# Kernel optimization log

Measured on AMD Instinct MI355X. Metric: run time of the kernel, lower is better.

## Reference

```python
import jax, jax.numpy as jnp
import numpy as np

S = 4  # upsample scale


def setup_inputs() -> dict:
    key = jax.random.key(0)
    ks = jax.random.split(key, 8)
    B, C, H, W = 4, 128, 64, 64
    feat_lr = jax.random.normal(ks[0], (B, C, H, W), dtype=jnp.float32)
    # gate: Conv2d(C, C//4, 1, bias=False) -> LeakyReLU(0.2) -> Conv2d(C//4, 1, 1, bias=True) -> Sigmoid
    gate_w1 = jax.random.normal(ks[1], (C, C // 4), dtype=jnp.float32) * 0.05
    gate_w2 = jax.random.normal(ks[2], (C // 4, 1), dtype=jnp.float32) * 0.1
    gate_b2 = jnp.full((1,), -3.0, dtype=jnp.float32)  # init bias per module
    # mlp: Conv2d(C+2, C, 1) -> ReLU -> Conv2d(C, C, 1)
    mlp_w1 = jax.random.normal(ks[3], (C + 2, C), dtype=jnp.float32) * 0.05
    mlp_b1 = jax.random.normal(ks[4], (C,), dtype=jnp.float32) * 0.01
    mlp_w2 = jax.random.normal(ks[5], (C, C), dtype=jnp.float32) * 0.05
    mlp_b2 = jax.random.normal(ks[6], (C,), dtype=jnp.float32) * 0.01
    return {"feat_lr": feat_lr, "gate_w1": gate_w1, "gate_w2": gate_w2,
            "gate_b2": gate_b2, "mlp_w1": mlp_w1, "mlp_b1": mlp_b1,
            "mlp_w2": mlp_w2, "mlp_b2": mlp_b2}


def reference(feat_lr, gate_w1, gate_w2, gate_b2, mlp_w1, mlp_b1, mlp_w2, mlp_b2):
    B, C, H, W = feat_lr.shape
    f = jnp.transpose(feat_lr, (0, 2, 3, 1))  # (B,H,W,C)

    # ---- gate on LR grid (1x1 convs == per-pixel matmuls) ----
    g = f @ gate_w1                              # (B,H,W,C//4)
    g = jnp.where(g >= 0, g, 0.2 * g)            # LeakyReLU(0.2)
    gate = jax.nn.sigmoid(g @ gate_w2 + gate_b2) # (B,H,W,1)

    # ---- subpixel grid: channels [x, y], values in (-1,1) ----
    coords = jnp.linspace(-1.0 + 1.0 / S, 1.0 - 1.0 / S, S, dtype=feat_lr.dtype)
    yy, xx = jnp.meshgrid(coords, coords, indexing="ij")
    grid = jnp.stack([xx, yy], axis=-1)          # (S,S,2)

    # ---- mlp: split first conv weight into feat part and grid part.
    # Since convs are 1x1 and feat_hr is nearest-upsampled (constant over each
    # SxS block) while grid tiles per block, hidden = relu(f@W1f + grid@W1g + b1)
    # broadcast over (block, subpixel) — avoids materializing concat/HR inputs.
    w1_f, w1_g = mlp_w1[:C], mlp_w1[C:]          # (C,C), (2,C)
    h_f = f @ w1_f                               # (B,H,W,C)
    h_g = grid @ w1_g                            # (S,S,C)
    hidden = jax.nn.relu(h_f[:, :, None, :, None, :]
                         + h_g[None, None, :, None, :, :]
                         + mlp_b1)               # (B,H,S,W,S,C)
    res = hidden @ mlp_w2 + mlp_b2               # (B,H,S,W,S,C)

    out = res * gate[:, :, None, :, None, :]     # broadcast gate over block
    out = out.reshape(B, H * S, W * S, C)
    return jnp.transpose(out, (0, 3, 1, 2))      # (B,C,H*S,W*S)
```

## Files before the change

kernel.cpp:

```cpp
#include <hip/hip_runtime.h>
#include <hip/hip_bf16.h>
#include <math.h>


typedef __attribute__((ext_vector_type(8))) short bf16x8;
typedef __attribute__((ext_vector_type(4))) float f32x4;

__device__ inline short f2bf(float v) {
    __hip_bfloat16 b = __float2bfloat16(v);
    return *reinterpret_cast<short*>(&b);
}

__device__ inline void barrier_lgkm() {
    asm volatile("s_waitcnt lgkmcnt(0)" ::: "memory");
    __builtin_amdgcn_s_barrier();
    asm volatile("" ::: "memory");
}

__global__ __launch_bounds__(256) void ipi_pre_kernel(
    const float* __restrict__ w2,
    const float* __restrict__ w1,
    const float* __restrict__ gw1,
    __hip_bfloat16* __restrict__ w2t,
    __hip_bfloat16* __restrict__ w1t_hi,
    __hip_bfloat16* __restrict__ w1t_lo,
    __hip_bfloat16* __restrict__ g1t_hi,
    __hip_bfloat16* __restrict__ g1t_lo)
{
    int gid = blockIdx.x * 256 + threadIdx.x;
    if (gid < 16384) {
        int j = gid >> 7, k = gid & 127;
        w2t[gid] = __float2bfloat16(w2[k * 128 + j]);
    } else if (gid < 32768) {
        int i = gid - 16384, j = i >> 7, c = i & 127;
        float v = w1[c * 128 + j];
        __hip_bfloat16 hi = __float2bfloat16(v);
        w1t_hi[i] = hi;
        w1t_lo[i] = __float2bfloat16(v - __bfloat162float(hi));
    } else if (gid < 36864) {
        int i = gid - 32768, jg = i >> 7, c = i & 127;
        float v = gw1[c * 32 + jg];
        __hip_bfloat16 hi = __float2bfloat16(v);
        g1t_hi[i] = hi;
        g1t_lo[i] = __float2bfloat16(v - __bfloat162float(hi));
    }
}

__global__ __launch_bounds__(256, 4) void ipi_main(
    const float* __restrict__ feat,
    const float* __restrict__ mlp_w1,
    const float* __restrict__ mlp_b1,
    const float* __restrict__ gate_w2,
    const float* __restrict__ gate_b2,
    const float* __restrict__ mlp_b2,
    const __hip_bfloat16* __restrict__ w2t,
    const __hip_bfloat16* __restrict__ w1t_hi,
    const __hip_bfloat16* __restrict__ w1t_lo,
    const __hip_bfloat16* __restrict__ g1t_hi,
    const __hip_bfloat16* __restrict__ g1t_lo,
    float* __restrict__ out)
{
    __shared__ float hf_s[16 * 132];
    __shared__ float hgb_s[16 * 132];
    __shared__ float gate_s[16];
    __shared__ char  hid[16384];
    short* f_hi = (short*)hid;
    short* f_lo = (short*)(hid + 4352);
    float* glds = (float*)(hid + 8704);

    const int t    = threadIdx.x;
    const int lane = t & 63;
    const int lg   = lane >> 4;
    const int ml   = lane & 15;
    const int wv   = t >> 6;
    const int bx   = blockIdx.x;
    const int w0   = (bx & 3) * 16;
    const int h    = (bx >> 2) & 63;
    const int b    = bx >> 8;

    bf16x8 afrag[2][4];
    f32x4  b2v[2];
    {
        const __hip_bfloat16* base = w2t + (wv * 32 + ml) * 128 + lg * 8;
        #pragma unroll
        for (int jt = 0; jt < 2; ++jt) {
            #pragma unroll
            for (int ks = 0; ks < 4; ++ks)
                afrag[jt][ks] = *(const bf16x8*)(base + jt * 2048 + ks * 32);
            b2v[jt] = *(const f32x4*)&mlp_b2[wv * 32 + jt * 16 + lg * 4];
        }
    }

    {
        const float* fbase = feat + ((size_t)(b * 128) * 64 + h) * 64 + w0;
        #pragma unroll
        for (int i = 0; i < 8; ++i) {
            int idx = t + i * 256;
            int c = idx >> 4, w = idx & 15;
            float v = fbase[(size_t)c * 4096 + w];
            short hi = f2bf(v);
            float hf32 = __bfloat162float(*(__hip_bfloat16*)&hi);
            f_hi[w * 136 + c] = hi;
            f_lo[w * 136 + c] = f2bf(v - hf32);
        }
        #pragma unroll
        for (int i = 0; i < 8; ++i) {
            int idx = t + i * 256;
            int s = idx >> 7, k = idx & 127;
            float cx = -0.75f + 0.5f * (float)(s & 3);
            float cy = -0.75f + 0.5f * (float)(s >> 2);
            hgb_s[s * 132 + k] = cx * mlp_w1[16384 + k]
                               + cy * mlp_w1[16512 + k] + mlp_b1[k];
        }
    }
    barrier_lgkm();

    {
        bf16x8 fhi[4], flo[4];
        {
            const short* fb  = f_hi + ml * 136 + lg * 8;
            const short* flb = f_lo + ml * 136 + lg * 8;
            #pragma unroll
            for (int ks = 0; ks < 4; ++ks) {
                fhi[ks] = *(const bf16x8*)(fb + ks * 32);
                flo[ks] = *(const bf16x8*)(flb + ks * 32);
            }
        }
        #pragma unroll
        for (int jj = 0; jj < 2; ++jj) {
            const int jt16 = (wv * 2 + jj) * 16;
            const __hip_bfloat16* bh = w1t_hi + (jt16 + ml) * 128 + lg * 8;
            const __hip_bfloat16* bl = w1t_lo + (jt16 + ml) * 128 + lg * 8;
            f32x4 acc = {0.f, 0.f, 0.f, 0.f};
            #pragma unroll
            for (int ks = 0; ks < 4; ++ks) {
                bf16x8 Bh = *(const bf16x8*)(bh + ks * 32);
                bf16x8 Bl = *(const bf16x8*)(bl + ks * 32);
                acc = __builtin_amdgcn_mfma_f32_16x16x32_bf16(fhi[ks], Bh, acc, 0, 0, 0);
                acc = __builtin_amdgcn_mfma_f32_16x16x32_bf16(fhi[ks], Bl, acc, 0, 0, 0);
                acc = __builtin_amdgcn_mfma_f32_16x16x32_bf16(flo[ks], Bh, acc, 0, 0, 0);
            }
            #pragma unroll
            for (int r = 0; r < 4; ++r)
                hf_s[(lg * 4 + r) * 132 + jt16 + ml] = acc[r];
        }
        if (wv == 0) {
            #pragma unroll
            for (int jt = 0; jt < 2; ++jt) {
                const __hip_bfloat16* bh = g1t_hi + (jt * 16 + ml) * 128 + lg * 8;
                const __hip_bfloat16* bl = g1t_lo + (jt * 16 + ml) * 128 + lg * 8;
                f32x4 acc = {0.f, 0.f, 0.f, 0.f};
                #pragma unroll
                for (int ks = 0; ks < 4; ++ks) {
                    bf16x8 Bh = *(const bf16x8*)(bh + ks * 32);
                    bf16x8 Bl = *(const bf16x8*)(bl + ks * 32);
                    acc = __builtin_amdgcn_mfma_f32_16x16x32_bf16(fhi[ks], Bh, acc, 0, 0, 0);
                    acc = __builtin_amdgcn_mfma_f32_16x16x32_bf16(fhi[ks], Bl, acc, 0, 0, 0);
                    acc = __builtin_amdgcn_mfma_f32_16x16x32_bf16(flo[ks], Bh, acc, 0, 0, 0);
                }
                #pragma unroll
                for (int r = 0; r < 4; ++r) {
                    float v = acc[r];
                    glds[(lg * 4 + r) * 33 + jt * 16 + ml] = (v >= 0.f) ? v : 0.2f * v;
                }
            }
        }
    }
    barrier_lgkm();

    if (t < 16) {
        float s = gate_b2[0];
        #pragma unroll 8
        for (int jg = 0; jg < 32; ++jg) s = fmaf(glds[t * 33 + jg], gate_w2[jg], s);
        gate_s[t] = 1.f / (1.f + expf(-s));
    }
    barrier_lgkm();

    const int mq  = t >> 2;
    const int wA  = mq >> 2;
    const int sxA = mq & 3;
    const int kq  = t & 3;
    for (int q = 0; q < 4; ++q) {
        {
            const float* hfr = hf_s  + wA * 132 + kq * 32;
            const float* hgr = hgb_s + (q * 4 + sxA) * 132 + kq * 32;
            char* rowp = hid + mq * 256;
            const int sw = (mq & 7) << 4;
            #pragma unroll
            for (int kc = 0; kc < 4; ++kc) {
                float4 a0 = *(const float4*)(hfr + kc * 8);
                float4 a1 = *(const float4*)(hfr + kc * 8 + 4);
                float4 g0 = *(const float4*)(hgr + kc * 8);
                float4 g1 = *(const float4*)(hgr + kc * 8 + 4);
                bf16x8 hv;
                hv[0] = f2bf(fmaxf(a0.x + g0.x, 0.f));
                hv[1] = f2bf(fmaxf(a0.y + g0.y, 0.f));
                hv[2] = f2bf(fmaxf(a0.z + g0.z, 0.f));
                hv[3] = f2bf(fmaxf(a0.w + g0.w, 0.f));
                hv[4] = f2bf(fmaxf(a1.x + g1.x, 0.f));
                hv[5] = f2bf(fmaxf(a1.y + g1.y, 0.f));
                hv[6] = f2bf(fmaxf(a1.z + g1.z, 0.f));
                hv[7] = f2bf(fmaxf(a1.w + g1.w, 0.f));
                *(bf16x8*)(rowp + ((kq * 64 + kc * 16) ^ sw)) = hv;
            }
        }
        barrier_lgkm();

        #pragma unroll
        for (int mt = 0; mt < 4; ++mt) {
            const int mrow = mt * 16 + ml;
            const int swb  = (mrow & 7) << 4;
            const char* rowp = hid + mrow * 256;
            bf16x8 bfrag[4];
            #pragma unroll
            for (int ks = 0; ks < 4; ++ks)
                bfrag[ks] = *(const bf16x8*)(rowp + ((ks * 64 + lg * 16) ^ swb));

            f32x4 acc0 = {0.f, 0.f, 0.f, 0.f};
            f32x4 acc1 = {0.f, 0.f, 0.f, 0.f};
            #pragma unroll
            for (int ks = 0; ks < 4; ++ks) {
                acc0 = __builtin_amdgcn_mfma_f32_16x16x32_bf16(afrag[0][ks], bfrag[ks], acc0, 0, 0, 0);
                acc1 = __builtin_amdgcn_mfma_f32_16x16x32_bf16(afrag[1][ks], bfrag[ks], acc1, 0, 0, 0);
            }

            const float g = gate_s[mrow >> 2];
            float* outp = out + ((size_t)(b * 128 + wv * 32 + lg * 4) << 16)
                              + (size_t)(h * 4 + q) * 256 + w0 * 4 + mrow;
            #pragma unroll
            for (int r = 0; r < 4; ++r) {
                outp[(size_t)r << 16]        = (acc0[r] + b2v[0][r]) * g;
                outp[(size_t)(r + 16) << 16] = (acc1[r] + b2v[1][r]) * g;
            }
        }
        barrier_lgkm();
    }
}

extern "C" void kernel_launch(void* const* d_in, const int* in_sizes, int n_in,
                              void* d_out, int out_size, void* d_ws, size_t ws_size,
                              hipStream_t stream) {
    const float* feat = (const float*)d_in[0];
    const float* gw1  = (const float*)d_in[1];
    const float* gw2  = (const float*)d_in[2];
    const float* gb2  = (const float*)d_in[3];
    const float* w1   = (const float*)d_in[4];
    const float* b1   = (const float*)d_in[5];
    const float* w2   = (const float*)d_in[6];
    const float* b2   = (const float*)d_in[7];
    float* o = (float*)d_out;

    char* ws = (char*)d_ws;
    __hip_bfloat16* w2t    = (__hip_bfloat16*)(ws);
    __hip_bfloat16* w1t_hi = (__hip_bfloat16*)(ws + 32768);
    __hip_bfloat16* w1t_lo = (__hip_bfloat16*)(ws + 65536);
    __hip_bfloat16* g1t_hi = (__hip_bfloat16*)(ws + 98304);
    __hip_bfloat16* g1t_lo = (__hip_bfloat16*)(ws + 106496);

    ipi_pre_kernel<<<dim3(144), dim3(256), 0, stream>>>(
        w2, w1, gw1, w2t, w1t_hi, w1t_lo, g1t_hi, g1t_lo);
    ipi_main<<<dim3(1024), dim3(256), 0, stream>>>(
        feat, w1, b1, gw2, gb2, b2, w2t, w1t_hi, w1t_lo, g1t_hi, g1t_lo, o);
}
```

Measured before the change: 44.36 us.

## Double-buffer hidden tile and overlap ReLU staging with MFMA chunks

```diff
diff --git a/kernel.cpp b/kernel.cpp
--- a/kernel.cpp
+++ b/kernel.cpp
@@ -91,6 +91,17 @@
         }
     }
 
+    float* ptrs[8];
+    {
+        float* pbase = out + ((size_t)(b * 128 + wv * 32 + lg * 4) << 16)
+                           + (size_t)(h * 4) * 256 + w0 * 4 + ml;
+        #pragma unroll
+        for (int jt = 0; jt < 2; ++jt)
+            #pragma unroll
+            for (int r = 0; r < 4; ++r)
+                ptrs[jt * 4 + r] = pbase + ((size_t)(jt * 16 + r) << 16);
+    }
+
     {
         const float* fbase = feat + ((size_t)(b * 128) * 64 + h) * 64 + w0;
         #pragma unroll
@@ -168,69 +179,81 @@
     }
     barrier_lgkm();
 
+    const int am = t & 31;
+    const int ak = t >> 5;
+    const int asw = (am & 7) << 4;
+    auto phaseA = [&](int c) {
+        const int gm = c * 32 + am;
+        const float* hfr = hf_s  + ((gm >> 2) & 15) * 132 + ak * 16;
+        const float* hgr = hgb_s + (((gm >> 6) << 2) | (gm & 3)) * 132 + ak * 16;
+        char* wp = hid + (c & 1) * 8192 + am * 256;
+        float4 a0 = *(const float4*)(hfr);
+        float4 a1 = *(const float4*)(hfr + 4);
+        float4 a2 = *(const float4*)(hfr + 8);
+        float4 a3 = *(const float4*)(hfr + 12);
+        float4 g0 = *(const float4*)(hgr);
+        float4 g1 = *(const float4*)(hgr + 4);
+        float4 g2 = *(const float4*)(hgr + 8);
+        float4 g3 = *(const float4*)(hgr + 12);
+        bf16x8 hv0, hv1;
+        hv0[0] = f2bf(fmaxf(a0.x + g0.x, 0.f));
+        hv0[1] = f2bf(fmaxf(a0.y + g0.y, 0.f));
+        hv0[2] = f2bf(fmaxf(a0.z + g0.z, 0.f));
+        hv0[3] = f2bf(fmaxf(a0.w + g0.w, 0.f));
+        hv0[4] = f2bf(fmaxf(a1.x + g1.x, 0.f));
+        hv0[5] = f2bf(fmaxf(a1.y + g1.y, 0.f));
+        hv0[6] = f2bf(fmaxf(a1.z + g1.z, 0.f));
+        hv0[7] = f2bf(fmaxf(a1.w + g1.w, 0.f));
+        hv1[0] = f2bf(fmaxf(a2.x + g2.x, 0.f));
+        hv1[1] = f2bf(fmaxf(a2.y + g2.y, 0.f));
+        hv1[2] = f2bf(fmaxf(a2.z + g2.z, 0.f));
+        hv1[3] = f2bf(fmaxf(a2.w + g2.w, 0.f));
+        hv1[4] = f2bf(fmaxf(a3.x + g3.x, 0.f));
+        hv1[5] = f2bf(fmaxf(a3.y + g3.y, 0.f));
+        hv1[6] = f2bf(fmaxf(a3.z + g3.z, 0.f));
+        hv1[7] = f2bf(fmaxf(a3.w + g3.w, 0.f));
+        *(bf16x8*)(wp + ((ak * 32) ^ asw))      = hv0;
+        *(bf16x8*)(wp + ((ak * 32 + 16) ^ asw)) = hv1;
+    };
+
     if (t < 16) {
         float s = gate_b2[0];
         #pragma unroll 8
         for (int jg = 0; jg < 32; ++jg) s = fmaf(glds[t * 33 + jg], gate_w2[jg], s);
         gate_s[t] = 1.f / (1.f + expf(-s));
     }
+    phaseA(0);
     barrier_lgkm();
 
-    const int mq  = t >> 2;
-    const int wA  = mq >> 2;
-    const int sxA = mq & 3;
-    const int kq  = t & 3;
-    for (int q = 0; q < 4; ++q) {
-        {
-            const float* hfr = hf_s  + wA * 132 + kq * 32;
-            const float* hgr = hgb_s + (q * 4 + sxA) * 132 + kq * 32;
-            char* rowp = hid + mq * 256;
-            const int sw = (mq & 7) << 4;
-            #pragma unroll
-            for (int kc = 0; kc < 4; ++kc) {
-                float4 a0 = *(const float4*)(hfr + kc * 8);
-                float4 a1 = *(const float4*)(hfr + kc * 8 + 4);
-                float4 g0 = *(const float4*)(hgr + kc * 8);
-                float4 g1 = *(const float4*)(hgr + kc * 8 + 4);
-                bf16x8 hv;
-                hv[0] = f2bf(fmaxf(a0.x + g0.x, 0.f));
-                hv[1] = f2bf(fmaxf(a0.y + g0.y, 0.f));
-                hv[2] = f2bf(fmaxf(a0.z + g0.z, 0.f));
-                hv[3] = f2bf(fmaxf(a0.w + g0.w, 0.f));
-                hv[4] = f2bf(fmaxf(a1.x + g1.x, 0.f));
-                hv[5] = f2bf(fmaxf(a1.y + g1.y, 0.f));
-                hv[6] = f2bf(fmaxf(a1.z + g1.z, 0.f));
-                hv[7] = f2bf(fmaxf(a1.w + g1.w, 0.f));
-                *(bf16x8*)(rowp + ((kq * 64 + kc * 16) ^ sw)) = hv;
-            }
-        }
-        barrier_lgkm();
-
-        #pragma unroll
-        for (int mt = 0; mt < 4; ++mt) {
-            const int mrow = mt * 16 + ml;
-            const int swb  = (mrow & 7) << 4;
-            const char* rowp = hid + mrow * 256;
+    #pragma unroll
+    for (int c = 0; c < 8; ++c) {
+        if (c < 7) phaseA(c + 1);
+
+        const char* buf = hid + (c & 1) * 8192;
+        #pragma unroll
+        for (int mt = 0; mt < 2; ++mt) {
+            const int row = mt * 16 + ml;
+            const int swb = (row & 7) << 4;
+            const char* rp = buf + row * 256;
             bf16x8 bfrag[4];
             #pragma unroll
             for (int ks = 0; ks < 4; ++ks)
-                bfrag[ks] = *(const bf16x8*)(rowp + ((ks * 64 + lg * 16) ^ swb));
-
-            f32x4 acc0 = {0.f, 0.f, 0.f, 0.f};
-            f32x4 acc1 = {0.f, 0.f, 0.f, 0.f};
+                bfrag[ks] = *(const bf16x8*)(rp + ((ks * 64 + lg * 16) ^ swb));
+
+            f32x4 acc0 = b2v[0];
+            f32x4 acc1 = b2v[1];
             #pragma unroll
             for (int ks = 0; ks < 4; ++ks) {
                 acc0 = __builtin_amdgcn_mfma_f32_16x16x32_bf16(afrag[0][ks], bfrag[ks], acc0, 0, 0, 0);
                 acc1 = __builtin_amdgcn_mfma_f32_16x16x32_bf16(afrag[1][ks], bfrag[ks], acc1, 0, 0, 0);
             }
 
-            const float g = gate_s[mrow >> 2];
-            float* outp = out + ((size_t)(b * 128 + wv * 32 + lg * 4) << 16)
-                              + (size_t)(h * 4 + q) * 256 + w0 * 4 + mrow;
+            const float g = gate_s[((c & 1) << 3) + (row >> 2)];
+            const int off = (c >> 1) * 256 + (c & 1) * 32 + mt * 16;
             #pragma unroll
             for (int r = 0; r < 4; ++r) {
-                outp[(size_t)r << 16]        = (acc0[r] + b2v[0][r]) * g;
-                outp[(size_t)(r + 16) << 16] = (acc1[r] + b2v[1][r]) * g;
+                ptrs[r][off]     = acc0[r] * g;
+                ptrs[4 + r][off] = acc1[r] * g;
             }
         }
         barrier_lgkm();
```

After: 47.11 us. 1.06x slower.

## Build hidden B-fragments in registers and keep all W2 fragments per wave

Applied to the files above, without the earlier changes.

```diff
diff --git a/kernel.cpp b/kernel.cpp
--- a/kernel.cpp
+++ b/kernel.cpp
@@ -9,6 +9,10 @@
 __device__ inline short f2bf(float v) {
     __hip_bfloat16 b = __float2bfloat16(v);
     return *reinterpret_cast<short*>(&b);
+}
+__device__ inline float bf2f(short s) {
+    __hip_bfloat16 b = *reinterpret_cast<__hip_bfloat16*>(&s);
+    return __bfloat162float(b);
 }
 
 __device__ inline void barrier_lgkm() {
@@ -46,7 +50,7 @@
     }
 }
 
-__global__ __launch_bounds__(256, 4) void ipi_main(
+__global__ __launch_bounds__(256, 2) void ipi_main(
     const float* __restrict__ feat,
     const float* __restrict__ mlp_w1,
     const float* __restrict__ mlp_b1,
@@ -60,13 +64,12 @@
     const __hip_bfloat16* __restrict__ g1t_lo,
     float* __restrict__ out)
 {
-    __shared__ float hf_s[16 * 132];
+    __shared__ short f_hi_s[16 * 136];
+    __shared__ short f_lo_s[16 * 136];
+    __shared__ short hf_s[16 * 144];
     __shared__ float hgb_s[16 * 132];
+    __shared__ float glds[16 * 33];
     __shared__ float gate_s[16];
-    __shared__ char  hid[16384];
-    short* f_hi = (short*)hid;
-    short* f_lo = (short*)(hid + 4352);
-    float* glds = (float*)(hid + 8704);
 
     const int t    = threadIdx.x;
     const int lane = t & 63;
@@ -78,19 +81,6 @@
     const int h    = (bx >> 2) & 63;
     const int b    = bx >> 8;
 
-    bf16x8 afrag[2][4];
-    f32x4  b2v[2];
-    {
-        const __hip_bfloat16* base = w2t + (wv * 32 + ml) * 128 + lg * 8;
-        #pragma unroll
-        for (int jt = 0; jt < 2; ++jt) {
-            #pragma unroll
-            for (int ks = 0; ks < 4; ++ks)
-                afrag[jt][ks] = *(const bf16x8*)(base + jt * 2048 + ks * 32);
-            b2v[jt] = *(const f32x4*)&mlp_b2[wv * 32 + jt * 16 + lg * 4];
-        }
-    }
-
     {
         const float* fbase = feat + ((size_t)(b * 128) * 64 + h) * 64 + w0;
         #pragma unroll
@@ -99,9 +89,8 @@
             int c = idx >> 4, w = idx & 15;
             float v = fbase[(size_t)c * 4096 + w];
             short hi = f2bf(v);
-            float hf32 = __bfloat162float(*(__hip_bfloat16*)&hi);
-            f_hi[w * 136 + c] = hi;
-            f_lo[w * 136 + c] = f2bf(v - hf32);
+            f_hi_s[w * 136 + c] = hi;
+            f_lo_s[w * 136 + c] = f2bf(v - bf2f(hi));
         }
         #pragma unroll
         for (int i = 0; i < 8; ++i) {
@@ -118,8 +107,8 @@
     {
         bf16x8 fhi[4], flo[4];
         {
-            const short* fb  = f_hi + ml * 136 + lg * 8;
-            const short* flb = f_lo + ml * 136 + lg * 8;
+            const short* fb  = f_hi_s + ml * 136 + lg * 8;
+            const short* flb = f_lo_s + ml * 136 + lg * 8;
             #pragma unroll
             for (int ks = 0; ks < 4; ++ks) {
                 fhi[ks] = *(const bf16x8*)(fb + ks * 32);
@@ -142,7 +131,7 @@
             }
             #pragma unroll
             for (int r = 0; r < 4; ++r)
-                hf_s[(lg * 4 + r) * 132 + jt16 + ml] = acc[r];
+                hf_s[(lg * 4 + r) * 144 + jt16 + ml] = f2bf(acc[r]);
         }
         if (wv == 0) {
             #pragma unroll
@@ -176,64 +165,64 @@
     }
     barrier_lgkm();
 
-    const int mq  = t >> 2;
-    const int wA  = mq >> 2;
-    const int sxA = mq & 3;
-    const int kq  = t & 3;
+    const int mloc = wv * 16 + ml;
+    const int w    = mloc >> 2;
+    const int sx   = mloc & 3;
+    const float g  = gate_s[w];
+
+    bf16x8 hfp[4];
+    #pragma unroll
+    for (int ks = 0; ks < 4; ++ks)
+        hfp[ks] = *(const bf16x8*)&hf_s[w * 144 + lg * 8 + ks * 32];
+
+    bf16x8 afrag[8][4];
+    #pragma unroll
+    for (int jt = 0; jt < 8; ++jt) {
+        const __hip_bfloat16* base = w2t + (jt * 16 + ml) * 128 + lg * 8;
+        #pragma unroll
+        for (int ks = 0; ks < 4; ++ks)
+            afrag[jt][ks] = *(const bf16x8*)(base + ks * 32);
+    }
+    f32x4 b2v[8];
+    #pragma unroll
+    for (int jt = 0; jt < 8; ++jt)
+        b2v[jt] = *(const f32x4*)&mlp_b2[jt * 16 + lg * 4];
+
+    float* pb = out + ((size_t)(b * 128 + lg * 4) << 16)
+                    + (size_t)(h * 4) * 256 + w0 * 4 + mloc;
+
+    #pragma unroll 1
     for (int q = 0; q < 4; ++q) {
-        {
-            const float* hfr = hf_s  + wA * 132 + kq * 32;
-            const float* hgr = hgb_s + (q * 4 + sxA) * 132 + kq * 32;
-            char* rowp = hid + mq * 256;
-            const int sw = (mq & 7) << 4;
-            #pragma unroll
-            for (int kc = 0; kc < 4; ++kc) {
-                float4 a0 = *(const float4*)(hfr + kc * 8);
-                float4 a1 = *(const float4*)(hfr + kc * 8 + 4);
-                float4 g0 = *(const float4*)(hgr + kc * 8);
-                float4 g1 = *(const float4*)(hgr + kc * 8 + 4);
-                bf16x8 hv;
-                hv[0] = f2bf(fmaxf(a0.x + g0.x, 0.f));
-                hv[1] = f2bf(fmaxf(a0.y + g0.y, 0.f));
-                hv[2] = f2bf(fmaxf(a0.z + g0.z, 0.f));
-                hv[3] = f2bf(fmaxf(a0.w + g0.w, 0.f));
-                hv[4] = f2bf(fmaxf(a1.x + g1.x, 0.f));
-                hv[5] = f2bf(fmaxf(a1.y + g1.y, 0.f));
-                hv[6] = f2bf(fmaxf(a1.z + g1.z, 0.f));
-                hv[7] = f2bf(fmaxf(a1.w + g1.w, 0.f));
-                *(bf16x8*)(rowp + ((kq * 64 + kc * 16) ^ sw)) = hv;
-            }
-        }
-        barrier_lgkm();
-
-        #pragma unroll
-        for (int mt = 0; mt < 4; ++mt) {
-            const int mrow = mt * 16 + ml;
-            const int swb  = (mrow & 7) << 4;
-            const char* rowp = hid + mrow * 256;
-            bf16x8 bfrag[4];
-            #pragma unroll
-            for (int ks = 0; ks < 4; ++ks)
-                bfrag[ks] = *(const bf16x8*)(rowp + ((ks * 64 + lg * 16) ^ swb));
-
-            f32x4 acc0 = {0.f, 0.f, 0.f, 0.f};
-            f32x4 acc1 = {0.f, 0.f, 0.f, 0.f};
-            #pragma unroll
-            for (int ks = 0; ks < 4; ++ks) {
-                acc0 = __builtin_amdgcn_mfma_f32_16x16x32_bf16(afrag[0][ks], bfrag[ks], acc0, 0, 0, 0);
-                acc1 = __builtin_amdgcn_mfma_f32_16x16x32_bf16(afrag[1][ks], bfrag[ks], acc1, 0, 0, 0);
-            }
-
-            const float g = gate_s[mrow >> 2];
-            float* outp = out + ((size_t)(b * 128 + wv * 32 + lg * 4) << 16)
-                              + (size_t)(h * 4 + q) * 256 + w0 * 4 + mrow;
-            #pragma unroll
-            for (int r = 0; r < 4; ++r) {
-                outp[(size_t)r << 16]        = (acc0[r] + b2v[0][r]) * g;
-                outp[(size_t)(r + 16) << 16] = (acc1[r] + b2v[1][r]) * g;
-            }
-        }
-        barrier_lgkm();
+        f32x4 acc[8];
+        #pragma unroll
+        for (int jt = 0; jt < 8; ++jt) acc[jt] = b2v[jt];
+
+        const float* hgr = hgb_s + (q * 4 + sx) * 132 + lg * 8;
+        #pragma unroll
+        for (int ks = 0; ks < 4; ++ks) {
+            float4 ga = *(const float4*)(hgr + ks * 32);
+            float4 gb = *(const float4*)(hgr + ks * 32 + 4);
+            bf16x8 bf;
+            bf[0] = f2bf(fmaxf(bf2f(hfp[ks][0]) + ga.x, 0.f));
+            bf[1] = f2bf(fmaxf(bf2f(hfp[ks][1]) + ga.y, 0.f));
+            bf[2] = f2bf(fmaxf(bf2f(hfp[ks][2]) + ga.z, 0.f));
+            bf[3] = f2bf(fmaxf(bf2f(hfp[ks][3]) + ga.w, 0.f));
+            bf[4] = f2bf(fmaxf(bf2f(hfp[ks][4]) + gb.x, 0.f));
+            bf[5] = f2bf(fmaxf(bf2f(hfp[ks][5]) + gb.y, 0.f));
+            bf[6] = f2bf(fmaxf(bf2f(hfp[ks][6]) + gb.z, 0.f));
+            bf[7] = f2bf(fmaxf(bf2f(hfp[ks][7]) + gb.w, 0.f));
+            #pragma unroll
+            for (int jt = 0; jt < 8; ++jt)
+                acc[jt] = __builtin_amdgcn_mfma_f32_16x16x32_bf16(afrag[jt][ks], bf, acc[jt], 0, 0, 0);
+        }
+
+        float* op = pb + q * 256;
+        #pragma unroll
+        for (int jt = 0; jt < 8; ++jt) {
+            #pragma unroll
+            for (int r = 0; r < 4; ++r)
+                op[(size_t)(jt * 16 + r) << 16] = acc[jt][r] * g;
+        }
     }
 }
 
```

New measurement: 65.08 us. 1.47x slower.
